# Kernel tuning notes

Measured on AMD Instinct MI355X. Metric: run time of the kernel, lower is better.

The kernel has to match this reference:

```python
import jax, jax.numpy as jnp
import numpy as np

B_, L_, DM = 2, 2048, 1024
DS, DC, EXP, HD = 128, 4, 2, 64
DI = EXP * DM              # 2048
NH = DI // HD              # 32 heads
CONV_DIM = DI + 2 * DS     # 2304
DIN = 2 * DI + 2 * DS + NH # 4384 (z, xBC, dt)
CS = 256                   # SSD chunk size
EPS = 1e-5


def setup_inputs() -> dict:
    key = jax.random.key(0)
    ks = jax.random.split(key, 8)
    s = 0.02
    x = jax.random.normal(ks[0], (B_, L_, DM), jnp.float32)
    norm_w = jnp.ones((DM,), jnp.float32)
    in_proj_w = jax.random.normal(ks[1], (DIN, DM), jnp.float32) * s
    conv_w = jax.random.normal(ks[2], (CONV_DIM, DC), jnp.float32) * 0.2
    conv_b = jnp.zeros((CONV_DIM,), jnp.float32)
    # inverse-softplus of dt ~ U(0.001, 0.1)
    dt_bias = jnp.log(jnp.expm1(jax.random.uniform(ks[3], (NH,), minval=0.001, maxval=0.1)))
    A_log = jnp.log(jax.random.uniform(ks[4], (NH,), minval=1.0, maxval=16.0))
    D = jnp.ones((NH,), jnp.float32)
    gnorm_w = jnp.ones((DI,), jnp.float32)
    out_proj_w = jax.random.normal(ks[5], (DM, DI), jnp.float32) * s
    return dict(x=x, norm_w=norm_w, in_proj_w=in_proj_w, conv_w=conv_w, conv_b=conv_b,
                dt_bias=dt_bias, A_log=A_log, D=D, gnorm_w=gnorm_w, out_proj_w=out_proj_w)


def _segsum(a):
    # a: [..., T] -> [..., T, T]; (i,j) = sum_{j<k<=i} a_k, -inf above diagonal
    T = a.shape[-1]
    cs = jnp.cumsum(a, -1)
    seg = cs[..., :, None] - cs[..., None, :]
    mask = jnp.tril(jnp.ones((T, T), bool))
    return jnp.where(mask, seg, -jnp.inf)


def _ssd(X, A, Bm, Cm):
    # X: [b,l,h,p] (= x*dt), A: [b,l,h] (= dt*a), Bm,Cm: [b,l,n] (ngroups=1)
    b, l, h, p = X.shape
    n, nc = Bm.shape[-1], l // CS
    X = X.reshape(b, nc, CS, h, p)
    A = A.reshape(b, nc, CS, h).transpose(0, 3, 1, 2)  # [b,h,c,s]
    Bm = Bm.reshape(b, nc, CS, n)
    Cm = Cm.reshape(b, nc, CS, n)
    Acs = jnp.cumsum(A, -1)                            # [b,h,c,s]
    Lmat = jnp.exp(_segsum(A))                         # [b,h,c,s,s]
    Y_diag = jnp.einsum('bcln,bcsn,bhcls,bcshp->bclhp', Cm, Bm, Lmat, X)
    decay_states = jnp.exp(Acs[..., -1:] - Acs)        # [b,h,c,s]
    states = jnp.einsum('bcln,bhcl,bclhp->bchpn', Bm, decay_states, X)
    states = jnp.concatenate([jnp.zeros_like(states[:, :1]), states], axis=1)  # [b,c+1,h,p,n]
    decay_chunk = jnp.exp(_segsum(jnp.pad(Acs[..., -1], ((0, 0), (0, 0), (1, 0)))))  # [b,h,c+1,c+1]
    states = jnp.einsum('bhzc,bchpn->bzhpn', decay_chunk, states)[:, :-1]
    Y_off = jnp.einsum('bcln,bchpn,bhcl->bclhp', Cm, states, jnp.exp(Acs))
    return (Y_diag + Y_off).reshape(b, l, h, p)


def _forward(x, norm_w, in_proj_w, conv_w, conv_b, dt_bias, A_log, D, gnorm_w, out_proj_w):
    b, l, _ = x.shape
    # outer RMSNorm
    xn = x * jax.lax.rsqrt(jnp.mean(x * x, -1, keepdims=True) + EPS) * norm_w
    zxbcdt = jnp.einsum('bld,ed->ble', xn, in_proj_w)
    z = zxbcdt[..., :DI]
    xBC = zxbcdt[..., DI:DI + CONV_DIM]
    dt = zxbcdt[..., -NH:]
    # causal depthwise conv1d + bias + silu
    pad = jnp.pad(xBC, ((0, 0), (DC - 1, 0), (0, 0)))
    conv = sum(pad[:, k:k + l, :] * conv_w[:, k] for k in range(DC)) + conv_b
    xBC = conv * jax.nn.sigmoid(conv)
    xs = xBC[..., :DI]
    Bm = xBC[..., DI:DI + DS]
    Cm = xBC[..., DI + DS:]
    dt = jax.nn.softplus(dt + dt_bias)                 # [b,l,h]
    A = -jnp.exp(A_log)                                # [h]
    xh = xs.reshape(b, l, NH, HD)
    y = _ssd(xh * dt[..., None], dt * A, Bm, Cm)
    y = y + D[None, None, :, None] * xh
    y = y.reshape(b, l, DI)
    # gated RMSNorm (norm_before_gate=False): rmsnorm(y * silu(z)) * w
    y = y * (z * jax.nn.sigmoid(z))
    y = y * jax.lax.rsqrt(jnp.mean(y * y, -1, keepdims=True) + EPS) * gnorm_w
    return x + jnp.einsum('bld,ed->ble', y, out_proj_w)


def reference(x, norm_w, in_proj_w, conv_w, conv_b, dt_bias, A_log, D, gnorm_w, out_proj_w):
    return _forward(x, norm_w, in_proj_w, conv_w, conv_b, dt_bias, A_log, D, gnorm_w, out_proj_w)
```

## Files before the change

### kernel.cpp

```cpp
#include <hip/hip_runtime.h>
#include <hip/hip_bf16.h>

#define BB      2
#define LSEQ    2048
#define DMODEL  1024
#define DSTATE  128
#define DCONV   4
#define HEADDIM 64
#define DINNER  2048
#define NHEADS  32
#define CONVD   2304
#define DINP    4384
#define NPAD_IN 4416
#define CHUNK   256
#define NCH     8
#define NROWS   4096
#define EPSF    1e-5f

typedef __attribute__((ext_vector_type(8))) short bf16x8;
typedef __attribute__((ext_vector_type(4))) float f32x4;

#define ASYNC_COPY16(gptr, lptr) \
    __builtin_amdgcn_global_load_lds((const __attribute__((address_space(1))) void*)(gptr), \
                                     (__attribute__((address_space(3))) void*)(lptr), 16, 0, 0)

__device__ __forceinline__ ushort f2bf(float f) {
    __hip_bfloat16 h = __float2bfloat16(f);
    return *(ushort*)&h;
}
__device__ __forceinline__ float bf2f(ushort u) {
    return __uint_as_float(((unsigned)u) << 16);
}
__device__ __forceinline__ short fb(float f) { return (short)f2bf(f); }

__global__ __launch_bounds__(256) void prologue_kernel(
    const float* __restrict__ x, const float* __restrict__ norm_w,
    const float* __restrict__ in_proj_w, const float* __restrict__ out_proj_w,
    ushort* __restrict__ xn_bf, ushort* __restrict__ wi_bf,
    ushort* __restrict__ wo_bf)
{
    int bid = blockIdx.x;
    if (bid < 4416) {
        long i4 = ((long)bid * 256 + threadIdx.x) * 4;
        int n = (int)(i4 >> 10);
        long k = i4 & 1023;
        ushort4 o;
        if (n < DINP) {
            float4 v = *(const float4*)(in_proj_w + ((long)n << 10) + k);
            o.x = f2bf(v.x); o.y = f2bf(v.y); o.z = f2bf(v.z); o.w = f2bf(v.w);
        } else { o.x = o.y = o.z = o.w = 0; }
        *(ushort4*)(wi_bf + i4) = o;
    } else if (bid < 6464) {
        long i4 = ((long)(bid - 4416) * 256 + threadIdx.x) * 4;
        float4 v = *(const float4*)(out_proj_w + i4);
        ushort4 o;
        o.x = f2bf(v.x); o.y = f2bf(v.y); o.z = f2bf(v.z); o.w = f2bf(v.w);
        *(ushort4*)(wo_bf + i4) = o;
    } else {
        int row = bid - 6464;
        const float* xr = x + (long)row * DMODEL;
        float4 v = *(const float4*)(xr + threadIdx.x * 4);
        float ss = v.x*v.x + v.y*v.y + v.z*v.z + v.w*v.w;
        for (int off = 32; off; off >>= 1) ss += __shfl_down(ss, off, 64);
        __shared__ float red[4];
        if ((threadIdx.x & 63) == 0) red[threadIdx.x >> 6] = ss;
        __syncthreads();
        float tot = red[0] + red[1] + red[2] + red[3];
        float scale = rsqrtf(tot / (float)DMODEL + EPSF);
        float4 wv = *(const float4*)(norm_w + threadIdx.x * 4);
        ushort4 o;
        o.x = f2bf(v.x * scale * wv.x); o.y = f2bf(v.y * scale * wv.y);
        o.z = f2bf(v.z * scale * wv.z); o.w = f2bf(v.w * scale * wv.w);
        *(ushort4*)(xn_bf + (long)row * DMODEL + threadIdx.x * 4) = o;
    }
}

__global__ __launch_bounds__(256, 4) void gemm_bf16_kernel(
    const ushort* __restrict__ A, int lda, long sA,
    const ushort* __restrict__ W, int ldw, long sW,
    void* __restrict__ Cout, int ldc, long sC, int c_bf16,
    const float* __restrict__ resid,
    int mtiles, int ntiles, int N, int K)
{
    __shared__ __align__(16) char smem[24576];
    ushort* As = (ushort*)smem;
    ushort* Bs = As + 128 * 64;
    ushort* tu = (ushort*)smem;
    float*  tf = (float*)smem;

    const int t = threadIdx.x;
    const int lane = t & 63;
    const int w = t >> 6;
    const int wm = w & 1, wn = w >> 1;
    const int lm = lane & 15, quad = lane >> 4;

    int pid = blockIdx.x;
    const int GM = 8;
    int width = GM * ntiles;
    int group = pid / width;
    int first_m = group * GM;
    int gsz = mtiles - first_m; if (gsz > GM) gsz = GM;
    int mt = first_m + (pid % width) % gsz;
    int nt = (pid % width) / gsz;
    const int m0 = mt * 128, n0 = nt * 64;

    A += (long)blockIdx.z * sA;
    W += (long)blockIdx.z * sW;

    const ushort* ga[4]; const ushort* gw[2];
#pragma unroll
    for (int i = 0; i < 4; ++i) {
        int s = i * 256 + t;
        int row = s >> 3;
        int kseg = (s & 7) ^ (row & 7);
        ga[i] = A + (long)(m0 + row) * lda + kseg * 8;
    }
#pragma unroll
    for (int i = 0; i < 2; ++i) {
        int s = i * 256 + t;
        int row = s >> 3;
        int kseg = (s & 7) ^ (row & 7);
        gw[i] = W + (long)(n0 + row) * ldw + kseg * 8;
    }

    f32x4 acc[4][2];
    f32x4 zero4 = {0.f, 0.f, 0.f, 0.f};
#pragma unroll
    for (int i = 0; i < 4; ++i) { acc[i][0] = zero4; acc[i][1] = zero4; }

    int arow8[4], arow7[4], brow8[2], brow7[2];
#pragma unroll
    for (int i = 0; i < 4; ++i) {
        int ar = wm * 64 + i * 16 + lm;
        arow8[i] = ar * 8; arow7[i] = ar & 7;
    }
#pragma unroll
    for (int i = 0; i < 2; ++i) {
        int br = wn * 32 + i * 16 + lm;
        brow8[i] = br * 8; brow7[i] = br & 7;
    }

    for (int k0 = 0; k0 < K; k0 += 64) {
#pragma unroll
        for (int i = 0; i < 4; ++i) {
            ASYNC_COPY16(ga[i], &As[(i * 256 + w * 64) * 8]);
            ga[i] += 64;
        }
#pragma unroll
        for (int i = 0; i < 2; ++i) {
            ASYNC_COPY16(gw[i], &Bs[(i * 256 + w * 64) * 8]);
            gw[i] += 64;
        }
        __syncthreads();
#pragma unroll
        for (int ks = 0; ks < 2; ++ks) {
            bf16x8 af[4], bfr[2];
#pragma unroll
            for (int i = 0; i < 4; ++i)
                af[i]  = *(const bf16x8*)&As[(arow8[i] + ((ks * 4 + quad) ^ arow7[i])) * 8];
#pragma unroll
            for (int i = 0; i < 2; ++i)
                bfr[i] = *(const bf16x8*)&Bs[(brow8[i] + ((ks * 4 + quad) ^ brow7[i])) * 8];
#pragma unroll
            for (int im = 0; im < 4; ++im)
#pragma unroll
                for (int in = 0; in < 2; ++in)
                    acc[im][in] = __builtin_amdgcn_mfma_f32_16x16x32_bf16(
                        af[im], bfr[in], acc[im][in], 0, 0, 0);
        }
        __syncthreads();
    }

    if (c_bf16) {
        ushort* C = (ushort*)Cout + (long)blockIdx.z * sC;
#pragma unroll
        for (int mi = 0; mi < 4; ++mi)
#pragma unroll
            for (int ni = 0; ni < 2; ++ni) {
                int c = wn * 32 + ni * 16 + lm;
#pragma unroll
                for (int i = 0; i < 4; ++i) {
                    int r = wm * 64 + mi * 16 + quad * 4 + i;
                    tu[r * 72 + c] = f2bf(acc[mi][ni][i]);
                }
            }
        __syncthreads();
        int r = t >> 1, cb = (t & 1) * 32;
        long rowbase = (long)(m0 + r) * ldc + n0 + cb;
#pragma unroll
        for (int q = 0; q < 4; ++q) {
            int gcol = n0 + cb + q * 8;
            if (gcol < N)
                *(bf16x8*)(C + rowbase + q * 8) =
                    *(const bf16x8*)&tu[r * 72 + cb + q * 8];
        }
    } else {
        float* C = (float*)Cout + (long)blockIdx.z * sC;
#pragma unroll
        for (int p = 0; p < 2; ++p) {
            if (wm == p) {
#pragma unroll
                for (int mi = 0; mi < 4; ++mi)
#pragma unroll
                    for (int ni = 0; ni < 2; ++ni) {
                        int c = wn * 32 + ni * 16 + lm;
#pragma unroll
                        for (int i = 0; i < 4; ++i) {
                            int r = mi * 16 + quad * 4 + i;
                            tf[r * 68 + c] = acc[mi][ni][i];
                        }
                    }
            }
            __syncthreads();
            int r2 = t >> 2, cb = (t & 3) * 16;
            long gbase = (long)(m0 + p * 64 + r2) * ldc + n0 + cb;
#pragma unroll
            for (int q = 0; q < 4; ++q) {
                float4 v = *(const float4*)&tf[r2 * 68 + cb + q * 4];
                if (resid) {
                    float4 rv = *(const float4*)(resid + gbase + q * 4);
                    v.x += rv.x; v.y += rv.y; v.z += rv.z; v.w += rv.w;
                }
                *(float4*)(C + gbase + q * 4) = v;
            }
            __syncthreads();
        }
    }
}

__global__ __launch_bounds__(256) void conv_acs_kernel(
    const ushort* __restrict__ zx, const float* __restrict__ cw,
    const float* __restrict__ cb, ushort* __restrict__ xBC_bf,
    const float* __restrict__ dt_bias, const float* __restrict__ A_log,
    float* __restrict__ dtv, float* __restrict__ Acs)
{
    int bid = blockIdx.x;
    if (bid < NROWS * 9) {
        int row = bid / 9;
        int c = (bid % 9) * 256 + threadIdx.x;
        int l = row & (LSEQ - 1);
        float acc = cb[c];
#pragma unroll
        for (int k = 0; k < DCONV; ++k) {
            int ls = l + k - (DCONV - 1);
            if (ls >= 0)
                acc += bf2f(zx[(long)(row + k - (DCONV - 1)) * DINP + DINNER + c]) * cw[c * DCONV + k];
        }
        xBC_bf[(long)row * CONVD + c] = f2bf(acc / (1.f + __expf(-acc)));
    } else {
        int idx = bid - NROWS * 9;
        int bc = idx >> 5, h = idx & 31;
        int l = threadIdx.x;
        int row = bc * CHUNK + l;
        float v = bf2f(zx[(long)row * DINP + (DINP - NHEADS) + h]) + dt_bias[h];
        float d = (v > 20.f) ? v : log1pf(__expf(v));
        dtv[row * NHEADS + h] = d;
        float a = -d * __expf(A_log[h]);
        __shared__ float buf[2][CHUNK];
        buf[0][l] = a; __syncthreads();
        int src = 0;
        for (int off = 1; off < CHUNK; off <<= 1) {
            float vv = buf[src][l];
            if (l >= off) vv += buf[src][l - off];
            buf[src ^ 1][l] = vv;
            __syncthreads();
            src ^= 1;
        }
        Acs[(bc * NHEADS + h) * CHUNK + l] = buf[src][l];
    }
}

#define XT_PAD 264
__global__ __launch_bounds__(256) void prep_transpose_kernel(
    const ushort* __restrict__ xBC_bf, const float* __restrict__ dtv,
    const float* __restrict__ acs, ushort* __restrict__ Xdt_t,
    ushort* __restrict__ Xcs_t, ushort* __restrict__ Bt)
{
    int bc = blockIdx.x, yt = blockIdx.y;
    int t = threadIdx.x;
    int row0 = bc * CHUNK;
    __shared__ ushort t_dt[64 * XT_PAD];
    __shared__ ushort t_cs[64 * XT_PAD];
    __shared__ float dl[CHUNK], cl[CHUNK];
    bool isB = (yt >= 32);
    int src_c0 = isB ? (DINNER + (yt - 32) * 64) : (yt * 64);
    if (!isB) {
        int h = yt;
        float a = acs[(bc * NHEADS + h) * CHUNK + t];
        float d = dtv[(row0 + t) * NHEADS + h];
        float T = acs[(bc * NHEADS + h) * CHUNK + CHUNK - 1];
        dl[t] = d;
        cl[t] = __expf(T - a) * d;
    }
    __syncthreads();
    for (int iter = 0; iter < 8; ++iter) {
        int l = iter * 32 + (t >> 3);
        int cc = (t & 7) * 8;
        ushort u[8];
        *(ushort4*)&u[0] = *(const ushort4*)(xBC_bf + (long)(row0 + l) * CONVD + src_c0 + cc);
        *(ushort4*)&u[4] = *(const ushort4*)(xBC_bf + (long)(row0 + l) * CONVD + src_c0 + cc + 4);
        if (isB) {
#pragma unroll
            for (int j = 0; j < 8; ++j) t_dt[(cc + j) * XT_PAD + l] = u[j];
        } else {
            float sd = dl[l], sc = cl[l];
#pragma unroll
            for (int j = 0; j < 8; ++j) {
                float f = bf2f(u[j]);
                t_dt[(cc + j) * XT_PAD + l] = f2bf(f * sd);
                t_cs[(cc + j) * XT_PAD + l] = f2bf(f * sc);
            }
        }
    }
    __syncthreads();
    int r = t >> 2, seg = (t & 3) * 64;
    const ushort* s1 = &t_dt[r * XT_PAD + seg];
    if (isB) {
        ushort* dst = Bt + ((long)bc * DSTATE + (yt - 32) * 64 + r) * CHUNK + seg;
#pragma unroll
        for (int q = 0; q < 16; ++q)
            *(ushort4*)(dst + q * 4) = *(const ushort4*)(s1 + q * 4);
    } else {
        const ushort* s2 = &t_cs[r * XT_PAD + seg];
        ushort* d1 = Xdt_t + ((long)bc * DINNER + yt * 64 + r) * CHUNK + seg;
        ushort* d2 = Xcs_t + ((long)bc * DINNER + yt * 64 + r) * CHUNK + seg;
#pragma unroll
        for (int q = 0; q < 16; ++q) {
            *(ushort4*)(d1 + q * 4) = *(const ushort4*)(s1 + q * 4);
            *(ushort4*)(d2 + q * 4) = *(const ushort4*)(s2 + q * 4);
        }
    }
}

__global__ __launch_bounds__(256) void chunk_state_mfma_kernel(
    const ushort* __restrict__ Xcs_t, const ushort* __restrict__ Bt,
    float* __restrict__ state_t)
{
    int bc = blockIdx.x, h = blockIdx.y;
    int t = threadIdx.x, lane = t & 63, w = t >> 6;
    int lm = lane & 15, quad = lane >> 4;
    const ushort* Xb = Xcs_t + ((long)bc * DINNER + h * HEADDIM) * CHUNK;
    const ushort* Bb = Bt + (long)bc * DSTATE * CHUNK;
    f32x4 acc[4][2];
    f32x4 zero4 = {0.f, 0.f, 0.f, 0.f};
#pragma unroll
    for (int i = 0; i < 4; ++i) { acc[i][0] = zero4; acc[i][1] = zero4; }

    for (int kt = 0; kt < 8; ++kt) {
        int k = kt * 32 + quad * 8;
        bf16x8 af[4], bfr[2];
#pragma unroll
        for (int mi = 0; mi < 4; ++mi)
            af[mi] = *(const bf16x8*)(Xb + (long)(mi * 16 + lm) * CHUNK + k);
#pragma unroll
        for (int nj = 0; nj < 2; ++nj)
            bfr[nj] = *(const bf16x8*)(Bb + (long)(w * 32 + nj * 16 + lm) * CHUNK + k);
#pragma unroll
        for (int mi = 0; mi < 4; ++mi)
#pragma unroll
            for (int nj = 0; nj < 2; ++nj)
                acc[mi][nj] = __builtin_amdgcn_mfma_f32_16x16x32_bf16(
                    af[mi], bfr[nj], acc[mi][nj], 0, 0, 0);
    }
    float* sp = state_t + (long)(bc * NHEADS + h) * (DSTATE * HEADDIM);
#pragma unroll
    for (int mi = 0; mi < 4; ++mi)
#pragma unroll
        for (int nj = 0; nj < 2; ++nj) {
            int n = w * 32 + nj * 16 + lm;
#pragma unroll
            for (int i = 0; i < 4; ++i) {
                int p = mi * 16 + quad * 4 + i;
                sp[p * DSTATE + n] = acc[mi][nj][i];
            }
        }
}

__global__ __launch_bounds__(256) void state_scan_kernel(
    float* __restrict__ state, const float* __restrict__ Acs)
{
    long flat = (long)blockIdx.x * 256 + threadIdx.x;
    int e = (int)(flat & 8191);
    int bh = (int)(flat >> 13);
    int b = bh >> 5, h = bh & 31;
    float S = 0.f;
    for (int c = 0; c < NCH; ++c) {
        int bc = b * NCH + c;
        long idx = ((long)(bc * NHEADS + h)) * 8192 + e;
        float T = Acs[(bc * NHEADS + h) * CHUNK + CHUNK - 1];
        float tmp = state[idx];
        state[idx] = S;
        S = S * __expf(T) + tmp;
    }
}

__global__ __launch_bounds__(256) void ssd_y_mfma_kernel(
    const ushort* __restrict__ xBC_bf, const ushort* __restrict__ Xdt_t,
    const ushort* __restrict__ G2b, const float* __restrict__ acs,
    const float* __restrict__ state_t, const ushort* __restrict__ zxb,
    const float* __restrict__ Dh, ushort* __restrict__ ybf)
{
    int bc = blockIdx.x, h = blockIdx.y;
    int t = threadIdx.x, lane = t & 63, w = t >> 6;
    int lm = lane & 15, quad = lane >> 4;
    int row0 = bc * CHUNK;
    __shared__ float acs_s[CHUNK];
    acs_s[t] = acs[(bc * NHEADS + h) * CHUNK + t];
    __syncthreads();
    int lbase = w * 64;
    float acs_l[4], eAl[4];
#pragma unroll
    for (int mi = 0; mi < 4; ++mi) {
        acs_l[mi] = acs_s[lbase + mi * 16 + lm];
        eAl[mi] = __expf(acs_l[mi]);
    }
    f32x4 acc[4][4];
    f32x4 zero4 = {0.f, 0.f, 0.f, 0.f};
#pragma unroll
    for (int i = 0; i < 4; ++i)
#pragma unroll
        for (int j = 0; j < 4; ++j) acc[i][j] = zero4;

    const ushort* Xb = Xdt_t + ((long)bc * DINNER + h * HEADDIM) * CHUNK;
    const ushort* g2 = G2b + (long)bc * (CHUNK * CHUNK);

    for (int ks = 0; ks <= 2 * w + 1; ++ks) {
        int sq = ks * 32 + quad * 8;
        bf16x8 bfr[4];
#pragma unroll
        for (int ni = 0; ni < 4; ++ni)
            bfr[ni] = *(const bf16x8*)(Xb + (long)(ni * 16 + lm) * CHUNK + sq);
        float a8[8];
#pragma unroll
        for (int j = 0; j < 8; ++j) a8[j] = acs_s[sq + j];
#pragma unroll
        for (int mi = 0; mi < 4; ++mi) {
            int lmin = lbase + mi * 16;
            if (ks * 32 > lmin + 15) continue;
            int lv = lmin + lm;
            float al = acs_l[mi];
            bf16x8 g8 = *(const bf16x8*)(g2 + (long)lv * CHUNK + sq);
            bf16x8 af;
#pragma unroll
            for (int j = 0; j < 8; ++j) {
                float v = bf2f((ushort)g8[j]) * __expf(al - a8[j]);
                af[j] = (sq + j > lv) ? (short)0 : fb(v);
            }
#pragma unroll
            for (int ni = 0; ni < 4; ++ni)
                acc[mi][ni] = __builtin_amdgcn_mfma_f32_16x16x32_bf16(
                    af, bfr[ni], acc[mi][ni], 0, 0, 0);
        }
    }

    const float* sp = state_t + (long)(bc * NHEADS + h) * (DSTATE * HEADDIM);
    const ushort* Cb = xBC_bf + (long)row0 * CONVD + DINNER + DSTATE;
    for (int kt = 0; kt < 4; ++kt) {
        int n0 = kt * 32 + quad * 8;
        bf16x8 bfr[4];
#pragma unroll
        for (int ni = 0; ni < 4; ++ni) {
            const float* s8 = sp + (ni * 16 + lm) * DSTATE + n0;
            f32x4 sA = *(const f32x4*)s8;
            f32x4 sB = *(const f32x4*)(s8 + 4);
            bf16x8 v;
#pragma unroll
            for (int j = 0; j < 4; ++j) { v[j] = fb(sA[j]); v[4 + j] = fb(sB[j]); }
            bfr[ni] = v;
        }
#pragma unroll
        for (int mi = 0; mi < 4; ++mi) {
            int lv = lbase + mi * 16 + lm;
            bf16x8 cu = *(const bf16x8*)(Cb + (long)lv * CONVD + n0);
            bf16x8 ce;
            float e = eAl[mi];
#pragma unroll
            for (int j = 0; j < 8; ++j) ce[j] = fb(bf2f((ushort)cu[j]) * e);
#pragma unroll
            for (int ni = 0; ni < 4; ++ni)
                acc[mi][ni] = __builtin_amdgcn_mfma_f32_16x16x32_bf16(
                    ce, bfr[ni], acc[mi][ni], 0, 0, 0);
        }
    }

    float Dv = Dh[h];
#pragma unroll
    for (int mi = 0; mi < 4; ++mi)
#pragma unroll
        for (int i = 0; i < 4; ++i) {
            int l = lbase + mi * 16 + quad * 4 + i;
            long row = row0 + l;
#pragma unroll
            for (int ni = 0; ni < 4; ++ni) {
                int p = ni * 16 + lm;
                float xh = bf2f(xBC_bf[row * CONVD + h * HEADDIM + p]);
                float z = bf2f(zxb[row * DINP + h * HEADDIM + p]);
                float o = (acc[mi][ni][i] + Dv * xh) * (z / (1.f + __expf(-z)));
                ybf[row * DINNER + h * HEADDIM + p] = f2bf(o);
            }
        }
}

__global__ __launch_bounds__(256) void gnorm_bf16_kernel(
    ushort* __restrict__ y, const float* __restrict__ gw)
{
    int row = blockIdx.x;
    ushort* yr = y + (long)row * DINNER;
    int base = threadIdx.x * 8;
    ushort4 a = *(ushort4*)(yr + base);
    ushort4 b = *(ushort4*)(yr + base + 4);
    float f[8] = {bf2f(a.x), bf2f(a.y), bf2f(a.z), bf2f(a.w),
                  bf2f(b.x), bf2f(b.y), bf2f(b.z), bf2f(b.w)};
    float ss = 0.f;
#pragma unroll
    for (int i = 0; i < 8; ++i) ss += f[i] * f[i];
    for (int off = 32; off; off >>= 1) ss += __shfl_down(ss, off, 64);
    __shared__ float red[4];
    if ((threadIdx.x & 63) == 0) red[threadIdx.x >> 6] = ss;
    __syncthreads();
    float tot = red[0] + red[1] + red[2] + red[3];
    float scale = rsqrtf(tot * (1.f / (float)DINNER) + EPSF);
    float4 g0 = *(const float4*)(gw + base);
    float4 g1 = *(const float4*)(gw + base + 4);
    ushort4 oa, ob;
    oa.x = f2bf(f[0] * scale * g0.x); oa.y = f2bf(f[1] * scale * g0.y);
    oa.z = f2bf(f[2] * scale * g0.z); oa.w = f2bf(f[3] * scale * g0.w);
    ob.x = f2bf(f[4] * scale * g1.x); ob.y = f2bf(f[5] * scale * g1.y);
    ob.z = f2bf(f[6] * scale * g1.z); ob.w = f2bf(f[7] * scale * g1.w);
    *(ushort4*)(yr + base) = oa;
    *(ushort4*)(yr + base + 4) = ob;
}

extern "C" void kernel_launch(void* const* d_in, const int* in_sizes, int n_in,
                              void* d_out, int out_size, void* d_ws, size_t ws_size,
                              hipStream_t stream)
{
    (void)in_sizes; (void)n_in; (void)out_size; (void)ws_size;
    const float* x          = (const float*)d_in[0];
    const float* norm_w     = (const float*)d_in[1];
    const float* in_proj_w  = (const float*)d_in[2];
    const float* conv_w     = (const float*)d_in[3];
    const float* conv_b     = (const float*)d_in[4];
    const float* dt_bias    = (const float*)d_in[5];
    const float* A_log      = (const float*)d_in[6];
    const float* Dh         = (const float*)d_in[7];
    const float* gnorm_w    = (const float*)d_in[8];
    const float* out_proj_w = (const float*)d_in[9];
    float* out = (float*)d_out;
    float* ws = (float*)d_ws;

    float* zxb_f   = ws;
    float* xbc_f   = zxb_f   + 8978432;
    float* dtv     = xbc_f   + 4718592;
    float* acs     = dtv     + 131072;
    float* g2_f    = acs     + 131072;
    float* state_t = g2_f    + 524288;
    float* xdt_f   = state_t + 4194304;
    float* xcs_f   = xdt_f   + 4194304;
    float* bt_f    = xcs_f   + 4194304;
    float* regU    = bt_f    + 262144;
    float* wo_f    = regU    + 4390912;

    ushort* zxb_bf = (ushort*)zxb_f;
    ushort* xBC_bf = (ushort*)xbc_f;
    ushort* G2b    = (ushort*)g2_f;
    ushort* Xdt_t  = (ushort*)xdt_f;
    ushort* Xcs_t  = (ushort*)xcs_f;
    ushort* Bt     = (ushort*)bt_f;
    ushort* xn_bf  = (ushort*)regU;
    ushort* wi_bf  = (ushort*)(regU + 2097152);
    ushort* ybf    = (ushort*)regU;
    ushort* wo_bf  = (ushort*)wo_f;

    prologue_kernel<<<dim3(10560), 256, 0, stream>>>(
        x, norm_w, in_proj_w, out_proj_w, xn_bf, wi_bf, wo_bf);

    gemm_bf16_kernel<<<dim3(32 * 69), 256, 0, stream>>>(
        xn_bf, DMODEL, 0, wi_bf, DMODEL, 0,
        zxb_bf, DINP, 0, 1, nullptr, 32, 69, DINP, DMODEL);

    conv_acs_kernel<<<dim3(NROWS * 9 + BB * NCH * NHEADS), 256, 0, stream>>>(
        zxb_bf, conv_w, conv_b, xBC_bf, dt_bias, A_log, dtv, acs);

    prep_transpose_kernel<<<dim3(BB * NCH, 34), 256, 0, stream>>>(
        xBC_bf, dtv, acs, Xdt_t, Xcs_t, Bt);

    gemm_bf16_kernel<<<dim3(8, 1, BB * NCH), 256, 0, stream>>>(
        xBC_bf + DINNER + DSTATE, CONVD, (long)CHUNK * CONVD,
        xBC_bf + DINNER, CONVD, (long)CHUNK * CONVD,
        G2b, CHUNK, (long)CHUNK * CHUNK, 1, nullptr, 2, 4, CHUNK, DSTATE);

    chunk_state_mfma_kernel<<<dim3(BB * NCH, NHEADS), 256, 0, stream>>>(
        Xcs_t, Bt, state_t);

    state_scan_kernel<<<dim3(BB * NHEADS * 8192 / 256), 256, 0, stream>>>(state_t, acs);

    ssd_y_mfma_kernel<<<dim3(BB * NCH, NHEADS), 256, 0, stream>>>(
        xBC_bf, Xdt_t, G2b, acs, state_t, zxb_bf, Dh, ybf);

    gnorm_bf16_kernel<<<dim3(NROWS), 256, 0, stream>>>(ybf, gnorm_w);

    gemm_bf16_kernel<<<dim3(32 * 16), 256, 0, stream>>>(
        ybf, DINNER, 0, wo_bf, DINNER, 0,
        out, DMODEL, 0, 0, x, 32, 16, DMODEL, DINNER);
}
```

Measured before the change: 332.0 us.

## Fuse gated RMSNorm into out-proj GEMM and transposes into SSD kernels

Removes the standalone gnorm kernel. Row sum-of-squares is now accumulated with atomics in the SSD output kernel, the rsqrt row scale is applied in the out-projection GEMM epilogue, and gnorm_w is folded into the bf16 out_proj weights during the prologue. The separate prep_transpose pass that wrote scaled X copies to global memory is dropped: the chunk-state and y kernels now transpose and scale the X tile in LDS themselves. Inter-chunk states are stored in bf16 instead of fp32, which halves that traffic but adds rounding in the state scan. The atomics add nondeterminism, and the sum of squares is taken from fp32 values before bf16 rounding.

```diff
diff --git a/kernel.cpp b/kernel.cpp
--- a/kernel.cpp
+++ b/kernel.cpp
@@ -16,6 +16,7 @@
 #define NCH     8
 #define NROWS   4096
 #define EPSF    1e-5f
+#define TPAD    264
 
 typedef __attribute__((ext_vector_type(8))) short bf16x8;
 typedef __attribute__((ext_vector_type(4))) float f32x4;
@@ -36,8 +37,9 @@
 __global__ __launch_bounds__(256) void prologue_kernel(
     const float* __restrict__ x, const float* __restrict__ norm_w,
     const float* __restrict__ in_proj_w, const float* __restrict__ out_proj_w,
+    const float* __restrict__ gnorm_w,
     ushort* __restrict__ xn_bf, ushort* __restrict__ wi_bf,
-    ushort* __restrict__ wo_bf)
+    ushort* __restrict__ wo_bf, float* __restrict__ ssq)
 {
     int bid = blockIdx.x;
     if (bid < 4416) {
@@ -52,11 +54,14 @@
         *(ushort4*)(wi_bf + i4) = o;
     } else if (bid < 6464) {
         long i4 = ((long)(bid - 4416) * 256 + threadIdx.x) * 4;
+        int k = (int)(i4 & 2047);
         float4 v = *(const float4*)(out_proj_w + i4);
+        float4 g = *(const float4*)(gnorm_w + k);
         ushort4 o;
-        o.x = f2bf(v.x); o.y = f2bf(v.y); o.z = f2bf(v.z); o.w = f2bf(v.w);
+        o.x = f2bf(v.x * g.x); o.y = f2bf(v.y * g.y);
+        o.z = f2bf(v.z * g.z); o.w = f2bf(v.w * g.w);
         *(ushort4*)(wo_bf + i4) = o;
-    } else {
+    } else if (bid < 10560) {
         int row = bid - 6464;
         const float* xr = x + (long)row * DMODEL;
         float4 v = *(const float4*)(xr + threadIdx.x * 4);
@@ -72,6 +77,8 @@
         o.x = f2bf(v.x * scale * wv.x); o.y = f2bf(v.y * scale * wv.y);
         o.z = f2bf(v.z * scale * wv.z); o.w = f2bf(v.w * scale * wv.w);
         *(ushort4*)(xn_bf + (long)row * DMODEL + threadIdx.x * 4) = o;
+    } else {
+        ssq[(bid - 10560) * 256 + threadIdx.x] = 0.f;
     }
 }
 
@@ -79,7 +86,7 @@
     const ushort* __restrict__ A, int lda, long sA,
     const ushort* __restrict__ W, int ldw, long sW,
     void* __restrict__ Cout, int ldc, long sC, int c_bf16,
-    const float* __restrict__ resid,
+    const float* __restrict__ resid, const float* __restrict__ rowscale,
     int mtiles, int ntiles, int N, int K)
 {
     __shared__ __align__(16) char smem[24576];
@@ -202,12 +209,15 @@
 #pragma unroll
                 for (int mi = 0; mi < 4; ++mi)
 #pragma unroll
-                    for (int ni = 0; ni < 2; ++ni) {
-                        int c = wn * 32 + ni * 16 + lm;
-#pragma unroll
-                        for (int i = 0; i < 4; ++i) {
-                            int r = mi * 16 + quad * 4 + i;
-                            tf[r * 68 + c] = acc[mi][ni][i];
+                    for (int i = 0; i < 4; ++i) {
+                        int r = mi * 16 + quad * 4 + i;
+                        float s = 1.f;
+                        if (rowscale)
+                            s = rsqrtf(rowscale[m0 + p * 64 + r] * (1.f / (float)DINNER) + EPSF);
+#pragma unroll
+                        for (int ni = 0; ni < 2; ++ni) {
+                            int c = wn * 32 + ni * 16 + lm;
+                            tf[r * 68 + c] = acc[mi][ni][i] * s;
                         }
                     }
             }
@@ -270,76 +280,62 @@
     }
 }
 
-#define XT_PAD 264
-__global__ __launch_bounds__(256) void prep_transpose_kernel(
-    const ushort* __restrict__ xBC_bf, const float* __restrict__ dtv,
-    const float* __restrict__ acs, ushort* __restrict__ Xdt_t,
-    ushort* __restrict__ Xcs_t, ushort* __restrict__ Bt)
-{
-    int bc = blockIdx.x, yt = blockIdx.y;
+__global__ __launch_bounds__(256) void prep_b_kernel(
+    const ushort* __restrict__ xBC_bf, ushort* __restrict__ Bt)
+{
+    int bc = blockIdx.x, half = blockIdx.y;
     int t = threadIdx.x;
     int row0 = bc * CHUNK;
-    __shared__ ushort t_dt[64 * XT_PAD];
-    __shared__ ushort t_cs[64 * XT_PAD];
-    __shared__ float dl[CHUNK], cl[CHUNK];
-    bool isB = (yt >= 32);
-    int src_c0 = isB ? (DINNER + (yt - 32) * 64) : (yt * 64);
-    if (!isB) {
-        int h = yt;
-        float a = acs[(bc * NHEADS + h) * CHUNK + t];
-        float d = dtv[(row0 + t) * NHEADS + h];
-        float T = acs[(bc * NHEADS + h) * CHUNK + CHUNK - 1];
-        dl[t] = d;
-        cl[t] = __expf(T - a) * d;
-    }
-    __syncthreads();
+    __shared__ ushort tB[64 * TPAD];
+    int src_c0 = DINNER + half * 64;
     for (int iter = 0; iter < 8; ++iter) {
         int l = iter * 32 + (t >> 3);
         int cc = (t & 7) * 8;
         ushort u[8];
         *(ushort4*)&u[0] = *(const ushort4*)(xBC_bf + (long)(row0 + l) * CONVD + src_c0 + cc);
         *(ushort4*)&u[4] = *(const ushort4*)(xBC_bf + (long)(row0 + l) * CONVD + src_c0 + cc + 4);
-        if (isB) {
-#pragma unroll
-            for (int j = 0; j < 8; ++j) t_dt[(cc + j) * XT_PAD + l] = u[j];
-        } else {
-            float sd = dl[l], sc = cl[l];
-#pragma unroll
-            for (int j = 0; j < 8; ++j) {
-                float f = bf2f(u[j]);
-                t_dt[(cc + j) * XT_PAD + l] = f2bf(f * sd);
-                t_cs[(cc + j) * XT_PAD + l] = f2bf(f * sc);
-            }
-        }
+#pragma unroll
+        for (int j = 0; j < 8; ++j) tB[(cc + j) * TPAD + l] = u[j];
     }
     __syncthreads();
     int r = t >> 2, seg = (t & 3) * 64;
-    const ushort* s1 = &t_dt[r * XT_PAD + seg];
-    if (isB) {
-        ushort* dst = Bt + ((long)bc * DSTATE + (yt - 32) * 64 + r) * CHUNK + seg;
-#pragma unroll
-        for (int q = 0; q < 16; ++q)
-            *(ushort4*)(dst + q * 4) = *(const ushort4*)(s1 + q * 4);
-    } else {
-        const ushort* s2 = &t_cs[r * XT_PAD + seg];
-        ushort* d1 = Xdt_t + ((long)bc * DINNER + yt * 64 + r) * CHUNK + seg;
-        ushort* d2 = Xcs_t + ((long)bc * DINNER + yt * 64 + r) * CHUNK + seg;
-#pragma unroll
-        for (int q = 0; q < 16; ++q) {
-            *(ushort4*)(d1 + q * 4) = *(const ushort4*)(s1 + q * 4);
-            *(ushort4*)(d2 + q * 4) = *(const ushort4*)(s2 + q * 4);
-        }
-    }
+    ushort* dst = Bt + ((long)bc * DSTATE + half * 64 + r) * CHUNK + seg;
+    const ushort* s1 = &tB[r * TPAD + seg];
+#pragma unroll
+    for (int q = 0; q < 16; ++q)
+        *(ushort4*)(dst + q * 4) = *(const ushort4*)(s1 + q * 4);
 }
 
 __global__ __launch_bounds__(256) void chunk_state_mfma_kernel(
-    const ushort* __restrict__ Xcs_t, const ushort* __restrict__ Bt,
-    float* __restrict__ state_t)
+    const ushort* __restrict__ xBC_bf, const ushort* __restrict__ Bt,
+    const float* __restrict__ dtv, const float* __restrict__ acs,
+    ushort* __restrict__ state)
 {
     int bc = blockIdx.x, h = blockIdx.y;
     int t = threadIdx.x, lane = t & 63, w = t >> 6;
     int lm = lane & 15, quad = lane >> 4;
-    const ushort* Xb = Xcs_t + ((long)bc * DINNER + h * HEADDIM) * CHUNK;
+    int row0 = bc * CHUNK;
+    __shared__ ushort xt[64 * TPAD];
+    __shared__ float cl[CHUNK];
+    {
+        float a = acs[(bc * NHEADS + h) * CHUNK + t];
+        float T = acs[(bc * NHEADS + h) * CHUNK + CHUNK - 1];
+        cl[t] = __expf(T - a) * dtv[(row0 + t) * NHEADS + h];
+    }
+    __syncthreads();
+    for (int iter = 0; iter < 8; ++iter) {
+        int l = iter * 32 + (t >> 3);
+        int cc = (t & 7) * 8;
+        ushort u[8];
+        *(ushort4*)&u[0] = *(const ushort4*)(xBC_bf + (long)(row0 + l) * CONVD + h * HEADDIM + cc);
+        *(ushort4*)&u[4] = *(const ushort4*)(xBC_bf + (long)(row0 + l) * CONVD + h * HEADDIM + cc + 4);
+        float sc = cl[l];
+#pragma unroll
+        for (int j = 0; j < 8; ++j)
+            xt[(cc + j) * TPAD + l] = f2bf(bf2f(u[j]) * sc);
+    }
+    __syncthreads();
+
     const ushort* Bb = Bt + (long)bc * DSTATE * CHUNK;
     f32x4 acc[4][2];
     f32x4 zero4 = {0.f, 0.f, 0.f, 0.f};
@@ -351,7 +347,7 @@
         bf16x8 af[4], bfr[2];
 #pragma unroll
         for (int mi = 0; mi < 4; ++mi)
-            af[mi] = *(const bf16x8*)(Xb + (long)(mi * 16 + lm) * CHUNK + k);
+            af[mi] = *(const bf16x8*)&xt[(mi * 16 + lm) * TPAD + k];
 #pragma unroll
         for (int nj = 0; nj < 2; ++nj)
             bfr[nj] = *(const bf16x8*)(Bb + (long)(w * 32 + nj * 16 + lm) * CHUNK + k);
@@ -362,7 +358,7 @@
                 acc[mi][nj] = __builtin_amdgcn_mfma_f32_16x16x32_bf16(
                     af[mi], bfr[nj], acc[mi][nj], 0, 0, 0);
     }
-    float* sp = state_t + (long)(bc * NHEADS + h) * (DSTATE * HEADDIM);
+    ushort* sp = state + (long)(bc * NHEADS + h) * (DSTATE * HEADDIM);
 #pragma unroll
     for (int mi = 0; mi < 4; ++mi)
 #pragma unroll
@@ -371,13 +367,13 @@
 #pragma unroll
             for (int i = 0; i < 4; ++i) {
                 int p = mi * 16 + quad * 4 + i;
-                sp[p * DSTATE + n] = acc[mi][nj][i];
+                sp[p * DSTATE + n] = f2bf(acc[mi][nj][i]);
             }
         }
 }
 
 __global__ __launch_bounds__(256) void state_scan_kernel(
-    float* __restrict__ state, const float* __restrict__ Acs)
+    ushort* __restrict__ state, const float* __restrict__ Acs)
 {
     long flat = (long)blockIdx.x * 256 + threadIdx.x;
     int e = (int)(flat & 8191);
@@ -388,25 +384,42 @@
         int bc = b * NCH + c;
         long idx = ((long)(bc * NHEADS + h)) * 8192 + e;
         float T = Acs[(bc * NHEADS + h) * CHUNK + CHUNK - 1];
-        float tmp = state[idx];
-        state[idx] = S;
+        float tmp = bf2f(state[idx]);
+        state[idx] = f2bf(S);
         S = S * __expf(T) + tmp;
     }
 }
 
 __global__ __launch_bounds__(256) void ssd_y_mfma_kernel(
-    const ushort* __restrict__ xBC_bf, const ushort* __restrict__ Xdt_t,
-    const ushort* __restrict__ G2b, const float* __restrict__ acs,
-    const float* __restrict__ state_t, const ushort* __restrict__ zxb,
-    const float* __restrict__ Dh, ushort* __restrict__ ybf)
+    const ushort* __restrict__ xBC_bf, const ushort* __restrict__ G2b,
+    const float* __restrict__ acs, const ushort* __restrict__ state,
+    const ushort* __restrict__ zxb, const float* __restrict__ dtv,
+    const float* __restrict__ Dh, ushort* __restrict__ ybf,
+    float* __restrict__ ssq)
 {
     int bc = blockIdx.x, h = blockIdx.y;
     int t = threadIdx.x, lane = t & 63, w = t >> 6;
     int lm = lane & 15, quad = lane >> 4;
     int row0 = bc * CHUNK;
+    __shared__ ushort xt[64 * TPAD];
     __shared__ float acs_s[CHUNK];
+    __shared__ float dl[CHUNK];
     acs_s[t] = acs[(bc * NHEADS + h) * CHUNK + t];
+    dl[t] = dtv[(row0 + t) * NHEADS + h];
     __syncthreads();
+    for (int iter = 0; iter < 8; ++iter) {
+        int l = iter * 32 + (t >> 3);
+        int cc = (t & 7) * 8;
+        ushort u[8];
+        *(ushort4*)&u[0] = *(const ushort4*)(xBC_bf + (long)(row0 + l) * CONVD + h * HEADDIM + cc);
+        *(ushort4*)&u[4] = *(const ushort4*)(xBC_bf + (long)(row0 + l) * CONVD + h * HEADDIM + cc + 4);
+        float sd = dl[l];
+#pragma unroll
+        for (int j = 0; j < 8; ++j)
+            xt[(cc + j) * TPAD + l] = f2bf(bf2f(u[j]) * sd);
+    }
+    __syncthreads();
+
     int lbase = w * 64;
     float acs_l[4], eAl[4];
 #pragma unroll
@@ -421,7 +434,6 @@
 #pragma unroll
         for (int j = 0; j < 4; ++j) acc[i][j] = zero4;
 
-    const ushort* Xb = Xdt_t + ((long)bc * DINNER + h * HEADDIM) * CHUNK;
     const ushort* g2 = G2b + (long)bc * (CHUNK * CHUNK);
 
     for (int ks = 0; ks <= 2 * w + 1; ++ks) {
@@ -429,7 +441,7 @@
         bf16x8 bfr[4];
 #pragma unroll
         for (int ni = 0; ni < 4; ++ni)
-            bfr[ni] = *(const bf16x8*)(Xb + (long)(ni * 16 + lm) * CHUNK + sq);
+            bfr[ni] = *(const bf16x8*)&xt[(ni * 16 + lm) * TPAD + sq];
         float a8[8];
 #pragma unroll
         for (int j = 0; j < 8; ++j) a8[j] = acs_s[sq + j];
@@ -453,21 +465,14 @@
         }
     }
 
-    const float* sp = state_t + (long)(bc * NHEADS + h) * (DSTATE * HEADDIM);
+    const ushort* sp = state + (long)(bc * NHEADS + h) * (DSTATE * HEADDIM);
     const ushort* Cb = xBC_bf + (long)row0 * CONVD + DINNER + DSTATE;
     for (int kt = 0; kt < 4; ++kt) {
         int n0 = kt * 32 + quad * 8;
         bf16x8 bfr[4];
 #pragma unroll
-        for (int ni = 0; ni < 4; ++ni) {
-            const float* s8 = sp + (ni * 16 + lm) * DSTATE + n0;
-            f32x4 sA = *(const f32x4*)s8;
-            f32x4 sB = *(const f32x4*)(s8 + 4);
-            bf16x8 v;
-#pragma unroll
-            for (int j = 0; j < 4; ++j) { v[j] = fb(sA[j]); v[4 + j] = fb(sB[j]); }
-            bfr[ni] = v;
-        }
+        for (int ni = 0; ni < 4; ++ni)
+            bfr[ni] = *(const bf16x8*)(sp + (long)(ni * 16 + lm) * DSTATE + n0);
 #pragma unroll
         for (int mi = 0; mi < 4; ++mi) {
             int lv = lbase + mi * 16 + lm;
@@ -490,45 +495,20 @@
         for (int i = 0; i < 4; ++i) {
             int l = lbase + mi * 16 + quad * 4 + i;
             long row = row0 + l;
+            float ps = 0.f;
 #pragma unroll
             for (int ni = 0; ni < 4; ++ni) {
                 int p = ni * 16 + lm;
                 float xh = bf2f(xBC_bf[row * CONVD + h * HEADDIM + p]);
                 float z = bf2f(zxb[row * DINP + h * HEADDIM + p]);
                 float o = (acc[mi][ni][i] + Dv * xh) * (z / (1.f + __expf(-z)));
+                ps += o * o;
                 ybf[row * DINNER + h * HEADDIM + p] = f2bf(o);
             }
-        }
-}
-
-__global__ __launch_bounds__(256) void gnorm_bf16_kernel(
-    ushort* __restrict__ y, const float* __restrict__ gw)
-{
-    int row = blockIdx.x;
-    ushort* yr = y + (long)row * DINNER;
-    int base = threadIdx.x * 8;
-    ushort4 a = *(ushort4*)(yr + base);
-    ushort4 b = *(ushort4*)(yr + base + 4);
-    float f[8] = {bf2f(a.x), bf2f(a.y), bf2f(a.z), bf2f(a.w),
-                  bf2f(b.x), bf2f(b.y), bf2f(b.z), bf2f(b.w)};
-    float ss = 0.f;
-#pragma unroll
-    for (int i = 0; i < 8; ++i) ss += f[i] * f[i];
-    for (int off = 32; off; off >>= 1) ss += __shfl_down(ss, off, 64);
-    __shared__ float red[4];
-    if ((threadIdx.x & 63) == 0) red[threadIdx.x >> 6] = ss;
-    __syncthreads();
-    float tot = red[0] + red[1] + red[2] + red[3];
-    float scale = rsqrtf(tot * (1.f / (float)DINNER) + EPSF);
-    float4 g0 = *(const float4*)(gw + base);
-    float4 g1 = *(const float4*)(gw + base + 4);
-    ushort4 oa, ob;
-    oa.x = f2bf(f[0] * scale * g0.x); oa.y = f2bf(f[1] * scale * g0.y);
-    oa.z = f2bf(f[2] * scale * g0.z); oa.w = f2bf(f[3] * scale * g0.w);
-    ob.x = f2bf(f[4] * scale * g1.x); ob.y = f2bf(f[5] * scale * g1.y);
-    ob.z = f2bf(f[6] * scale * g1.z); ob.w = f2bf(f[7] * scale * g1.w);
-    *(ushort4*)(yr + base) = oa;
-    *(ushort4*)(yr + base + 4) = ob;
+#pragma unroll
+            for (int m = 1; m < 16; m <<= 1) ps += __shfl_xor(ps, m, 64);
+            if (lm == 0) atomicAdd(&ssq[row], ps);
+        }
 }
 
 extern "C" void kernel_launch(void* const* d_in, const int* in_sizes, int n_in,
@@ -554,53 +534,48 @@
     float* dtv     = xbc_f   + 4718592;
     float* acs     = dtv     + 131072;
     float* g2_f    = acs     + 131072;
-    float* state_t = g2_f    + 524288;
-    float* xdt_f   = state_t + 4194304;
-    float* xcs_f   = xdt_f   + 4194304;
-    float* bt_f    = xcs_f   + 4194304;
+    float* state_f = g2_f    + 524288;
+    float* bt_f    = state_f + 2097152;
     float* regU    = bt_f    + 262144;
     float* wo_f    = regU    + 4390912;
+    float* ssq     = wo_f    + 1048576;
 
     ushort* zxb_bf = (ushort*)zxb_f;
     ushort* xBC_bf = (ushort*)xbc_f;
     ushort* G2b    = (ushort*)g2_f;
-    ushort* Xdt_t  = (ushort*)xdt_f;
-    ushort* Xcs_t  = (ushort*)xcs_f;
+    ushort* state  = (ushort*)state_f;
     ushort* Bt     = (ushort*)bt_f;
     ushort* xn_bf  = (ushort*)regU;
     ushort* wi_bf  = (ushort*)(regU + 2097152);
     ushort* ybf    = (ushort*)regU;
     ushort* wo_bf  = (ushort*)wo_f;
 
-    prologue_kernel<<<dim3(10560), 256, 0, stream>>>(
-        x, norm_w, in_proj_w, out_proj_w, xn_bf, wi_bf, wo_bf);
+    prologue_kernel<<<dim3(10576), 256, 0, stream>>>(
+        x, norm_w, in_proj_w, out_proj_w, gnorm_w, xn_bf, wi_bf, wo_bf, ssq);
 
     gemm_bf16_kernel<<<dim3(32 * 69), 256, 0, stream>>>(
         xn_bf, DMODEL, 0, wi_bf, DMODEL, 0,
-        zxb_bf, DINP, 0, 1, nullptr, 32, 69, DINP, DMODEL);
+        zxb_bf, DINP, 0, 1, nullptr, nullptr, 32, 69, DINP, DMODEL);
 
     conv_acs_kernel<<<dim3(NROWS * 9 + BB * NCH * NHEADS), 256, 0, stream>>>(
         zxb_bf, conv_w, conv_b, xBC_bf, dt_bias, A_log, dtv, acs);
 
-    prep_transpose_kernel<<<dim3(BB * NCH, 34), 256, 0, stream>>>(
-        xBC_bf, dtv, acs, Xdt_t, Xcs_t, Bt);
+    prep_b_kernel<<<dim3(BB * NCH, 2), 256, 0, stream>>>(xBC_bf, Bt);
 
     gemm_bf16_kernel<<<dim3(8, 1, BB * NCH), 256, 0, stream>>>(
         xBC_bf + DINNER + DSTATE, CONVD, (long)CHUNK * CONVD,
         xBC_bf + DINNER, CONVD, (long)CHUNK * CONVD,
-        G2b, CHUNK, (long)CHUNK * CHUNK, 1, nullptr, 2, 4, CHUNK, DSTATE);
+        G2b, CHUNK, (long)CHUNK * CHUNK, 1, nullptr, nullptr, 2, 4, CHUNK, DSTATE);
 
     chunk_state_mfma_kernel<<<dim3(BB * NCH, NHEADS), 256, 0, stream>>>(
-        Xcs_t, Bt, state_t);
-
-    state_scan_kernel<<<dim3(BB * NHEADS * 8192 / 256), 256, 0, stream>>>(state_t, acs);
+        xBC_bf, Bt, dtv, acs, state);
+
+    state_scan_kernel<<<dim3(BB * NHEADS * 8192 / 256), 256, 0, stream>>>(state, acs);
 
     ssd_y_mfma_kernel<<<dim3(BB * NCH, NHEADS), 256, 0, stream>>>(
-        xBC_bf, Xdt_t, G2b, acs, state_t, zxb_bf, Dh, ybf);
-
-    gnorm_bf16_kernel<<<dim3(NROWS), 256, 0, stream>>>(ybf, gnorm_w);
+        xBC_bf, G2b, acs, state, zxb_bf, dtv, Dh, ybf, ssq);
 
     gemm_bf16_kernel<<<dim3(32 * 16), 256, 0, stream>>>(
         ybf, DINNER, 0, wo_bf, DINNER, 0,
-        out, DMODEL, 0, 0, x, 32, 16, DMODEL, DINNER);
-}
+        out, DMODEL, 0, 0, x, ssq, 32, 16, DMODEL, DINNER);
+}
```

Measured after the change: 305.6 us. -7.9%, faster.
